# Kernel tuning notes

Measured on AMD Instinct MI355X. Metric: run time of the kernel, lower is better.

Reference implementation:

```python
import jax, jax.numpy as jnp
import numpy as np

DIM = 1280
HEADS = 16
HEAD_DIM = DIM // HEADS  # 80
N_CHUNKS = 8
CHUNK = 1024
TOTAL = N_CHUNKS * CHUNK  # 8192 packed tokens


def rotate_half(x):
    x1, x2 = jnp.split(x, 2, axis=-1)
    return jnp.concatenate([-x2, x1], axis=-1)


def setup_inputs() -> dict:
    key = jax.random.key(0)
    k0, k1, k2 = jax.random.split(key, 3)
    hidden_states = jax.random.normal(k0, (TOTAL, DIM), dtype=jnp.float32)
    # 2D-rope style per-token angles, duplicated halves (standard vision RoPE layout)
    inv_freq = 1.0 / (10000.0 ** (jnp.arange(0, HEAD_DIM, 2, dtype=jnp.float32) / HEAD_DIM))
    pos = jnp.arange(TOTAL, dtype=jnp.float32)
    freqs = pos[:, None] * inv_freq[None, :]            # [T, HEAD_DIM//2]
    emb = jnp.concatenate([freqs, freqs], axis=-1)      # [T, HEAD_DIM]
    cos = jnp.cos(emb)
    sin = jnp.sin(emb)
    qkv_w = jax.random.normal(k1, (3 * DIM, DIM), dtype=jnp.float32) * 0.02
    qkv_b = jnp.zeros((3 * DIM,), dtype=jnp.float32)
    proj_w = jax.random.normal(k2, (DIM, DIM), dtype=jnp.float32) * 0.02
    proj_b = jnp.zeros((DIM,), dtype=jnp.float32)
    cu_seqlens = (jnp.arange(N_CHUNKS + 1, dtype=jnp.int32) * CHUNK)
    return {"hidden_states": hidden_states, "cos": cos, "sin": sin,
            "qkv_w": qkv_w, "qkv_b": qkv_b, "proj_w": proj_w, "proj_b": proj_b,
            "cu_seqlens": cu_seqlens}


def reference(hidden_states, cos, sin, qkv_w, qkv_b, proj_w, proj_b, cu_seqlens):
    # Equal-length chunks (cu_seqlens uniform): vectorize the Python chunk loop
    # as a leading batch axis n over chunks of length L.
    n = cu_seqlens.shape[0] - 1
    total, dim = hidden_states.shape
    L = total // n
    scaling = HEAD_DIM ** -0.5

    x = hidden_states.reshape(n, L, dim)
    qkv = x @ qkv_w.T + qkv_b                              # [n, L, 3*dim]
    qkv = qkv.reshape(n, L, 3, HEADS, HEAD_DIM)
    q, k, v = qkv[:, :, 0], qkv[:, :, 1], qkv[:, :, 2]     # [n, L, H, hd]

    # inline RoPE in fp32 (matches apply_rotary_pos_emb_vision)
    c = cos.reshape(n, L, 1, HEAD_DIM).astype(jnp.float32)
    s = sin.reshape(n, L, 1, HEAD_DIM).astype(jnp.float32)
    qf = q.astype(jnp.float32)
    kf = k.astype(jnp.float32)
    q = (qf * c + rotate_half(qf) * s).astype(q.dtype)
    k = (kf * c + rotate_half(kf) * s).astype(k.dtype)

    # naive per-chunk full attention: QK^T, fp32 softmax, PV
    scores = jnp.einsum('nlhd,nmhd->nhlm', q, k) * scaling  # [n, H, L, L]
    probs = jax.nn.softmax(scores.astype(jnp.float32), axis=-1).astype(q.dtype)
    out = jnp.einsum('nhlm,nmhd->nlhd', probs, v)           # [n, L, H, hd]
    out = out.reshape(n, L, dim)
    out = out @ proj_w.T + proj_b                           # [n, L, dim]
    return out.reshape(total, dim)
```

## Files before the change

kernel.cpp:

```cpp
#include <hip/hip_runtime.h>
#include <stdint.h>

#define DIM 1280
#define HEADS 16
#define HD 80
#define TOTAL 8192
#define CHUNK 1024
#define QKVN 3840

typedef __attribute__((ext_vector_type(8))) __bf16 bf16x8;
typedef __attribute__((ext_vector_type(4))) float floatx4;

typedef __attribute__((address_space(1))) const uint32_t gu32;
typedef __attribute__((address_space(3))) uint32_t lu32;

__device__ __forceinline__ void llds16(const void* g, void* l) {
  __builtin_amdgcn_global_load_lds((gu32*)g, (lu32*)l, 16, 0, 0);
}

__device__ __forceinline__ unsigned short f2b(float f) {
  union { __bf16 b; unsigned short u; } x; x.b = (__bf16)f; return x.u;
}
__device__ __forceinline__ float b2f(unsigned short u) {
  union { __bf16 b; unsigned short u; } x; x.u = u; return (float)x.b;
}
__device__ __forceinline__ float fexp2(float x) {
#if __has_builtin(__builtin_amdgcn_exp2f)
  return __builtin_amdgcn_exp2f(x);
#else
  return __expf(x * 0.6931471805599453f);
#endif
}

#define QSCALE (0.11180339887498949f * 1.44269504088896340f)

#define QROW 96
#define KT_SH (64 * 104)
#define VT_SH (80 * 72)

__global__ void cvt_bf16(const float* __restrict__ src, unsigned short* __restrict__ dst, int n4) {
  int i = blockIdx.x * 256 + threadIdx.x;
  if (i >= n4) return;
  float4 v = reinterpret_cast<const float4*>(src)[i];
  ushort4 o;
  o.x = f2b(v.x); o.y = f2b(v.y); o.z = f2b(v.z); o.w = f2b(v.w);
  reinterpret_cast<ushort4*>(dst)[i] = o;
}


__device__ __forceinline__ void stage_a64(const unsigned short* __restrict__ G,
                                          unsigned short* ls, int wv, int lane,
                                          int row0, int kk, int hi) {
#pragma unroll
  for (int t = 0; t < 2; ++t) {
    const int stripe = t * 8 + wv;
    const int rb = ((stripe >> 3) << 7) + ((stripe & 7) << 3) + hi;
    const int r = rb + (lane >> 3);
    const int ch = (lane & 7) ^ (r & 7);
    llds16(G + (size_t)(row0 + r) * DIM + kk + (ch << 3), ls + rb * 64);
  }
}

__device__ __forceinline__ void stage_b64(const unsigned short* __restrict__ G,
                                          unsigned short* ls, int wv, int lane,
                                          int row0, int kk, int hi) {
#pragma unroll
  for (int t = 0; t < 2; ++t) {
    const int stripe = t * 8 + wv;
    const int rb = ((stripe >> 2) << 6) + ((stripe & 3) << 3) + hi;
    const int r = rb + (lane >> 3);
    const int ch = (lane & 7) ^ (r & 7);
    llds16(G + (size_t)(row0 + r) * DIM + kk + (ch << 3), ls + rb * 64);
  }
}

__device__ __forceinline__ bf16x8 frg(const unsigned short* ls, int r, int cx) {
  return *reinterpret_cast<const bf16x8*>(ls + r * 64 + (cx << 3));
}

#define MFMA_BF16 __builtin_amdgcn_mfma_f32_16x16x32_bf16
#define LGKM0() asm volatile("s_waitcnt lgkmcnt(0)" ::: "memory")
#define BARR()  asm volatile("s_barrier" ::: "memory")

template<int MODE>
__launch_bounds__(512, 2)
__global__ void gemm8(const unsigned short* __restrict__ A,
                      const unsigned short* __restrict__ B,
                      const float* __restrict__ bias,
                      unsigned short* __restrict__ qo,
                      unsigned short* __restrict__ ko,
                      unsigned short* __restrict__ vo,
                      float* __restrict__ fo) {
  __shared__ __attribute__((aligned(16))) unsigned short lsA[2][256 * 64];
  __shared__ __attribute__((aligned(16))) unsigned short lsB[2][256 * 64];
  const int m0 = blockIdx.x * 256;
  const int n0 = blockIdx.y * 256;
  const int tid = threadIdx.x;
  const int wv = tid >> 6, lane = tid & 63;
  const int wr = wv >> 2, wc = wv & 3;
  const int q4 = lane >> 4, l15 = lane & 15;
  const int sx = l15 & 7;
  const int cx0 = q4 ^ sx;
  const int cx1 = (4 + q4) ^ sx;

  stage_a64(A, &lsA[0][0], wv, lane, m0, 0, 0);
  stage_b64(B, &lsB[0][0], wv, lane, n0, 0, 0);
  stage_b64(B, &lsB[0][0], wv, lane, n0, 0, 32);
  stage_a64(A, &lsA[0][0], wv, lane, m0, 0, 64);
  stage_b64(B, &lsB[1][0], wv, lane, n0, 64, 0);
  stage_a64(A, &lsA[1][0], wv, lane, m0, 64, 0);
  stage_b64(B, &lsB[1][0], wv, lane, n0, 64, 32);

  floatx4 acc[8][4];
#pragma unroll
  for (int i = 0; i < 8; ++i)
#pragma unroll
    for (int j = 0; j < 4; ++j)
      acc[i][j] = (floatx4){0.f, 0.f, 0.f, 0.f};

  asm volatile("s_waitcnt vmcnt(6)" ::: "memory");
  BARR();

  const int rA = wr * 128 + l15;
  const int rB = wc * 64 + l15;

  bf16x8 ArLo[4][2], ArHi[4][2], Blo[2][2], Bhi[2][2];

#pragma unroll 2
  for (int kt = 0; kt < 20; ++kt) {
    const unsigned short* la = &lsA[kt & 1][0];
    const unsigned short* lb = &lsB[kt & 1][0];
    unsigned short* aN = &lsA[(kt & 1) ^ 1][0];
    unsigned short* aC = &lsA[kt & 1][0];
    unsigned short* bC = &lsB[kt & 1][0];
    const bool st1 = (kt + 1 < 20);
    const bool st2 = (kt + 2 < 20);

    if (kt > 0) {
#pragma unroll
      for (int m = 0; m < 4; ++m)
#pragma unroll
        for (int n = 0; n < 2; ++n) {
          acc[m + 4][n] = MFMA_BF16(ArHi[m][0], Blo[n][0], acc[m + 4][n], 0, 0, 0);
          acc[m + 4][n] = MFMA_BF16(ArHi[m][1], Blo[n][1], acc[m + 4][n], 0, 0, 0);
        }
    }
#pragma unroll
    for (int m = 0; m < 4; ++m) {
      ArLo[m][0] = frg(la, rA + m * 16, cx0);
      ArLo[m][1] = frg(la, rA + m * 16, cx1);
    }
#pragma unroll
    for (int n = 0; n < 2; ++n) {
      Blo[n][0] = frg(lb, rB + n * 16, cx0);
      Blo[n][1] = frg(lb, rB + n * 16, cx1);
    }
    if (st1) stage_a64(A, aN, wv, lane, m0, (kt + 1) * 64, 64);
    LGKM0();
    BARR();

#pragma unroll
    for (int m = 0; m < 4; ++m)
#pragma unroll
      for (int n = 0; n < 2; ++n) {
        acc[m][n] = MFMA_BF16(ArLo[m][0], Blo[n][0], acc[m][n], 0, 0, 0);
        acc[m][n] = MFMA_BF16(ArLo[m][1], Blo[n][1], acc[m][n], 0, 0, 0);
      }
#pragma unroll
    for (int n = 0; n < 2; ++n) {
      Bhi[n][0] = frg(lb, rB + (n + 2) * 16, cx0);
      Bhi[n][1] = frg(lb, rB + (n + 2) * 16, cx1);
    }
    if (st2) stage_b64(B, bC, wv, lane, n0, (kt + 2) * 64, 0);
    LGKM0();
    BARR();

#pragma unroll
    for (int m = 0; m < 4; ++m)
#pragma unroll
      for (int n = 0; n < 2; ++n) {
        acc[m][n + 2] = MFMA_BF16(ArLo[m][0], Bhi[n][0], acc[m][n + 2], 0, 0, 0);
        acc[m][n + 2] = MFMA_BF16(ArLo[m][1], Bhi[n][1], acc[m][n + 2], 0, 0, 0);
      }
#pragma unroll
    for (int m = 0; m < 4; ++m) {
      ArHi[m][0] = frg(la, rA + (m + 4) * 16, cx0);
      ArHi[m][1] = frg(la, rA + (m + 4) * 16, cx1);
    }
    if (st2) stage_a64(A, aC, wv, lane, m0, (kt + 2) * 64, 0);
    LGKM0();
    BARR();

#pragma unroll
    for (int m = 0; m < 4; ++m)
#pragma unroll
      for (int n = 0; n < 2; ++n) {
        acc[m + 4][n + 2] = MFMA_BF16(ArHi[m][0], Bhi[n][0], acc[m + 4][n + 2], 0, 0, 0);
        acc[m + 4][n + 2] = MFMA_BF16(ArHi[m][1], Bhi[n][1], acc[m + 4][n + 2], 0, 0, 0);
      }
    if (st2) stage_b64(B, bC, wv, lane, n0, (kt + 2) * 64, 32);
    if (st2)      asm volatile("s_waitcnt vmcnt(6)" ::: "memory");
    else if (st1) asm volatile("s_waitcnt vmcnt(0)" ::: "memory");
    BARR();
  }

#pragma unroll
  for (int m = 0; m < 4; ++m)
#pragma unroll
    for (int n = 0; n < 2; ++n) {
      acc[m + 4][n] = MFMA_BF16(ArHi[m][0], Blo[n][0], acc[m + 4][n], 0, 0, 0);
      acc[m + 4][n] = MFMA_BF16(ArHi[m][1], Blo[n][1], acc[m + 4][n], 0, 0, 0);
    }

  unsigned short* os = nullptr;
  int nloc = n0;
  if (MODE == 0) {
    if (blockIdx.y < 5)       { os = qo; }
    else if (blockIdx.y < 10) { os = ko; nloc = n0 - DIM; }
    else                      { os = vo; nloc = n0 - 2 * DIM; }
  }
#pragma unroll
  for (int n = 0; n < 4; ++n) {
    const int cg = wc * 64 + n * 16 + l15;
    const float bn = bias[n0 + cg];
#pragma unroll
    for (int m = 0; m < 8; ++m) {
#pragma unroll
      for (int r = 0; r < 4; ++r) {
        const int row = m0 + wr * 128 + m * 16 + q4 * 4 + r;
        const float val = acc[m][n][r] + bn;
        if (MODE == 0) os[(size_t)row * DIM + nloc + cg] = f2b(val);
        else           fo[(size_t)row * DIM + n0 + cg] = val;
      }
    }
  }
}

__global__ void prep_q(const unsigned short* __restrict__ qbuf,
                       const float* __restrict__ cp, const float* __restrict__ sp,
                       unsigned short* __restrict__ qimg) {
  const int m = blockIdx.x, tid = threadIdx.x;
  const int ch = m >> 10, rl = m & 1023;
#pragma unroll
  for (int i = 0; i < 3; ++i) {
    const int it = i * 256 + tid;
    if (it < 640) {
      const int h = it / 40, d = it - h * 40;
      const float c = cp[m * HD + d], s = sp[m * HD + d];
      const float x1 = b2f(qbuf[(size_t)m * DIM + h * HD + d]);
      const float x2 = b2f(qbuf[(size_t)m * DIM + h * HD + d + 40]);
      const size_t ob = ((size_t)(ch * 16 + h) * 1024 + rl) * QROW;
      qimg[ob + d]      = f2b((x1 * c - x2 * s) * QSCALE);
      qimg[ob + d + 40] = f2b((x2 * c + x1 * s) * QSCALE);
    }
  }
  { const int h = tid >> 4, c = tid & 15;
    qimg[((size_t)(ch * 16 + h) * 1024 + rl) * QROW + 80 + c] = 0; }
}

__global__ void prep_k(const unsigned short* __restrict__ kbuf,
                       const float* __restrict__ cp, const float* __restrict__ sp,
                       unsigned short* __restrict__ kimg) {
  const int m = blockIdx.x, tid = threadIdx.x;
  const int ch = m >> 10, rl = m & 1023;
  const int jt = rl >> 6, rr = rl & 63;
#pragma unroll
  for (int i = 0; i < 3; ++i) {
    const int it = i * 256 + tid;
    if (it < 640) {
      const int h = it / 40, d = it - h * 40;
      const float c = cp[m * HD + d], s = sp[m * HD + d];
      const float x1 = b2f(kbuf[(size_t)m * DIM + h * HD + d]);
      const float x2 = b2f(kbuf[(size_t)m * DIM + h * HD + d + 40]);
      const size_t ob = ((size_t)((ch * 16 + h) * 16 + jt) * KT_SH) + rr * 104;
      kimg[ob + d]      = f2b(x1 * c - x2 * s);
      kimg[ob + d + 40] = f2b(x2 * c + x1 * s);
    }
  }
#pragma unroll
  for (int i = 0; i < 2; ++i) {
    const int it = i * 256 + tid;
    if (it < 384) {
      const int h = it / 24, c = it - h * 24;
      kimg[((size_t)((ch * 16 + h) * 16 + jt) * KT_SH) + rr * 104 + 80 + c] = 0;
    }
  }
}

__global__ void prep_v(const unsigned short* __restrict__ vbuf,
                       unsigned short* __restrict__ vimg) {
  __shared__ __attribute__((aligned(16))) unsigned short lsT[64 * 88];
  const int bx = blockIdx.x;
  const int jt = bx & 15, h = (bx >> 4) & 15, ch = bx >> 8;
  const int tid = threadIdx.x;
  const int row0 = ch * CHUNK + jt * 64;
#pragma unroll
  for (int i = 0; i < 3; ++i) {
    const int it = i * 256 + tid;
    if (it < 640) {
      const int r = it / 10, c = it - r * 10;
      const uint4 v = *reinterpret_cast<const uint4*>(vbuf + (size_t)(row0 + r) * DIM + h * HD + c * 8);
      *reinterpret_cast<uint4*>(&lsT[r * 88 + c * 8]) = v;
    }
  }
  __syncthreads();
  unsigned short* ot = vimg + (size_t)((ch * 16 + h) * 16 + jt) * VT_SH;
#pragma unroll
  for (int i = 0; i < 12; ++i) {
    const int it = i * 256 + tid;
    if (it < 2880) {
      const int d = it / 36, kk = it - d * 36;
      uint32_t w = 0;
      if (kk < 32) {
        const uint32_t lo = lsT[(2 * kk) * 88 + d];
        const uint32_t hi = lsT[(2 * kk + 1) * 88 + d];
        w = lo | (hi << 16);
      }
      *reinterpret_cast<uint32_t*>(ot + d * 72 + kk * 2) = w;
    }
  }
}

__launch_bounds__(256, 3)
__global__ void attn_k(const unsigned short* __restrict__ qimg,
                       const unsigned short* __restrict__ kimg,
                       const unsigned short* __restrict__ vimg,
                       unsigned short* __restrict__ ob) {
  __shared__ __attribute__((aligned(16))) unsigned short lsK[KT_SH];
  __shared__ __attribute__((aligned(16))) unsigned short lsV[VT_SH];
  __shared__ __attribute__((aligned(16))) unsigned short lsP[128 * 72];

  const int bx = blockIdx.x;
  const int qt = bx & 7, h = (bx >> 3) & 15, ch = bx >> 7;
  const int tid = threadIdx.x, wv = tid >> 6, lane = tid & 63;
  const int q4 = lane >> 4, l15 = lane & 15;
  const int qrow_loc = qt * 128 + wv * 32;

  bf16x8 aq[2][3];
  {
    const unsigned short* qb = qimg + ((size_t)(ch * 16 + h) * 1024 + qrow_loc) * QROW;
#pragma unroll
    for (int mt = 0; mt < 2; ++mt)
#pragma unroll
      for (int ks = 0; ks < 3; ++ks)
        aq[mt][ks] = *reinterpret_cast<const bf16x8*>(qb + (size_t)(mt * 16 + l15) * QROW + ks * 32 + q4 * 8);
  }

  floatx4 oacc[2][5];
  float lpart[2] = {0.f, 0.f};
#pragma unroll
  for (int mt = 0; mt < 2; ++mt)
#pragma unroll
    for (int t = 0; t < 5; ++t) oacc[mt][t] = (floatx4){0.f, 0.f, 0.f, 0.f};

  const char* kbase = (const char*)(kimg + (size_t)(ch * 16 + h) * 16 * KT_SH);
  const char* vbase = (const char*)(vimg + (size_t)(ch * 16 + h) * 16 * VT_SH);

  for (int jt = 0; jt < 16; ++jt) {
    __syncthreads();
    {
      const char* kg = kbase + (size_t)jt * (KT_SH * 2);
#pragma unroll
      for (int r = 0; r < 4; ++r) {
        const int off = (r * 4 + wv) * 1024;
        if (off < KT_SH * 2)
          llds16(kg + off + lane * 16, (char*)lsK + off);
      }
      const char* vg = vbase + (size_t)jt * (VT_SH * 2);
#pragma unroll
      for (int r = 0; r < 3; ++r) {
        const int off = (r * 4 + wv) * 1024;
        if (off < VT_SH * 2) {
          if (off + 1024 <= VT_SH * 2) llds16(vg + off + lane * 16, (char*)lsV + off);
          else if (lane < 16)          llds16(vg + off + lane * 16, (char*)lsV + off);
        }
      }
    }
    __syncthreads();

    floatx4 sfr[2][4];
#pragma unroll
    for (int c = 0; c < 4; ++c) {
      const bf16x8 ak0 = *reinterpret_cast<const bf16x8*>(&lsK[(c * 16 + l15) * 104 + 0  + q4 * 8]);
      const bf16x8 ak1 = *reinterpret_cast<const bf16x8*>(&lsK[(c * 16 + l15) * 104 + 32 + q4 * 8]);
      const bf16x8 ak2 = *reinterpret_cast<const bf16x8*>(&lsK[(c * 16 + l15) * 104 + 64 + q4 * 8]);
#pragma unroll
      for (int mt = 0; mt < 2; ++mt) {
        floatx4 s = (floatx4){0.f, 0.f, 0.f, 0.f};
        s = __builtin_amdgcn_mfma_f32_16x16x32_bf16(ak0, aq[mt][0], s, 0, 0, 0);
        s = __builtin_amdgcn_mfma_f32_16x16x32_bf16(ak1, aq[mt][1], s, 0, 0, 0);
        s = __builtin_amdgcn_mfma_f32_16x16x32_bf16(ak2, aq[mt][2], s, 0, 0, 0);
        sfr[mt][c] = s;
      }
    }

#pragma unroll
    for (int mt = 0; mt < 2; ++mt)
#pragma unroll
      for (int c = 0; c < 4; ++c) {
        const float p0 = fexp2(sfr[mt][c][0]);
        const float p1 = fexp2(sfr[mt][c][1]);
        const float p2 = fexp2(sfr[mt][c][2]);
        const float p3 = fexp2(sfr[mt][c][3]);
        lpart[mt] += (p0 + p1) + (p2 + p3);
        ushort4 w;
        w.x = f2b(p0); w.y = f2b(p1); w.z = f2b(p2); w.w = f2b(p3);
        *reinterpret_cast<ushort4*>(&lsP[(wv * 32 + mt * 16 + l15) * 72 + c * 16 + q4 * 4]) = w;
      }

#pragma unroll
    for (int ks = 0; ks < 2; ++ks) {
      const bf16x8 ap0 = *reinterpret_cast<const bf16x8*>(&lsP[(wv * 32 + 0  + l15) * 72 + ks * 32 + q4 * 8]);
      const bf16x8 ap1 = *reinterpret_cast<const bf16x8*>(&lsP[(wv * 32 + 16 + l15) * 72 + ks * 32 + q4 * 8]);
#pragma unroll
      for (int t = 0; t < 5; ++t) {
        const bf16x8 bv = *reinterpret_cast<const bf16x8*>(&lsV[(t * 16 + l15) * 72 + ks * 32 + q4 * 8]);
        oacc[0][t] = __builtin_amdgcn_mfma_f32_16x16x32_bf16(ap0, bv, oacc[0][t], 0, 0, 0);
        oacc[1][t] = __builtin_amdgcn_mfma_f32_16x16x32_bf16(ap1, bv, oacc[1][t], 0, 0, 0);
      }
    }
  }

#pragma unroll
  for (int mt = 0; mt < 2; ++mt) {
    lpart[mt] += __shfl_xor(lpart[mt], 16, 64);
    lpart[mt] += __shfl_xor(lpart[mt], 32, 64);
  }
  float inv[2];
  inv[0] = 1.0f / lpart[0];
  inv[1] = 1.0f / lpart[1];

  float invr[2][4];
#pragma unroll
  for (int mt = 0; mt < 2; ++mt)
#pragma unroll
    for (int r = 0; r < 4; ++r)
      invr[mt][r] = __shfl(inv[mt], q4 * 4 + r, 64);

#pragma unroll
  for (int mt = 0; mt < 2; ++mt)
#pragma unroll
    for (int t = 0; t < 5; ++t)
#pragma unroll
      for (int r = 0; r < 4; ++r) {
        const int gr = ch * CHUNK + qrow_loc + mt * 16 + q4 * 4 + r;
        const int gc = h * HD + t * 16 + l15;
        ob[(size_t)gr * DIM + gc] = f2b(oacc[mt][t][r] * invr[mt][r]);
      }
}

extern "C" void kernel_launch(void* const* d_in, const int* in_sizes, int n_in,
                              void* d_out, int out_size, void* d_ws, size_t ws_size,
                              hipStream_t stream) {
  (void)in_sizes; (void)n_in; (void)out_size; (void)ws_size;
  const float* hs    = (const float*)d_in[0];
  const float* cosp  = (const float*)d_in[1];
  const float* sinp  = (const float*)d_in[2];
  const float* qkvw  = (const float*)d_in[3];
  const float* qkvb  = (const float*)d_in[4];
  const float* projw = (const float*)d_in[5];
  const float* projb = (const float*)d_in[6];

  char* ws = (char*)d_ws;
  unsigned short* xb   = (unsigned short*)(ws + 0);
  unsigned short* wq   = (unsigned short*)(ws + 20971520);
  unsigned short* qbuf = (unsigned short*)(ws + 30801920);
  unsigned short* kbuf = (unsigned short*)(ws + 51773440);
  unsigned short* vbuf = (unsigned short*)(ws + 72744960);
  unsigned short* wp   = (unsigned short*)(ws + 93716480);
  unsigned short* obuf = (unsigned short*)(ws + 96993280);
  unsigned short* kimg = (unsigned short*)(ws + 117964800);
  unsigned short* qimg = (unsigned short*)(ws + 0);
  unsigned short* vimg = (unsigned short*)(ws + 30801920);

  cvt_bf16<<<TOTAL * DIM / 4 / 256, 256, 0, stream>>>(hs, xb, TOTAL * DIM / 4);
  cvt_bf16<<<QKVN * DIM / 4 / 256, 256, 0, stream>>>(qkvw, wq, QKVN * DIM / 4);
  cvt_bf16<<<DIM * DIM / 4 / 256, 256, 0, stream>>>(projw, wp, DIM * DIM / 4);

  gemm8<0><<<dim3(TOTAL / 256, QKVN / 256), 512, 0, stream>>>(
      xb, wq, qkvb, qbuf, kbuf, vbuf, nullptr);

  prep_q<<<TOTAL, 256, 0, stream>>>(qbuf, cosp, sinp, qimg);
  prep_k<<<TOTAL, 256, 0, stream>>>(kbuf, cosp, sinp, kimg);
  prep_v<<<2048, 256, 0, stream>>>(vbuf, vimg);

  attn_k<<<1024, 256, 0, stream>>>(qimg, kimg, vimg, obuf);

  gemm8<1><<<dim3(TOTAL / 256, DIM / 256), 512, 0, stream>>>(
      obuf, wp, projb, nullptr, nullptr, nullptr, (float*)d_out);
}
```

Baseline: 351.4 us.

## Double-buffer K/V tiles in attention and raise wave priority around MFMAs

The attention kernel now keeps two LDS buffers for K and V. It issues the async global-to-LDS load for the next key tile right after the barrier, then computes on the current tile, and drops the second barrier per iteration. MFMA sections are wrapped in s_setprio to favour matrix issue. The doubled LDS footprint lowers the launch-bounds occupancy hint from 3 to 2 blocks. The compiler may also insert conservative vmcnt waits before the LDS reads, which would cancel much of the intended overlap.

```diff
diff --git a/kernel.cpp b/kernel.cpp
--- a/kernel.cpp
+++ b/kernel.cpp
@@ -321,13 +321,13 @@
   }
 }
 
-__launch_bounds__(256, 3)
+__launch_bounds__(256, 2)
 __global__ void attn_k(const unsigned short* __restrict__ qimg,
                        const unsigned short* __restrict__ kimg,
                        const unsigned short* __restrict__ vimg,
                        unsigned short* __restrict__ ob) {
-  __shared__ __attribute__((aligned(16))) unsigned short lsK[KT_SH];
-  __shared__ __attribute__((aligned(16))) unsigned short lsV[VT_SH];
+  __shared__ __attribute__((aligned(16))) unsigned short lsK[2][KT_SH];
+  __shared__ __attribute__((aligned(16))) unsigned short lsV[2][VT_SH];
   __shared__ __attribute__((aligned(16))) unsigned short lsP[128 * 72];
 
   const int bx = blockIdx.x;
@@ -356,34 +356,43 @@
   const char* kbase = (const char*)(kimg + (size_t)(ch * 16 + h) * 16 * KT_SH);
   const char* vbase = (const char*)(vimg + (size_t)(ch * 16 + h) * 16 * VT_SH);
 
+  auto stage_kv = [&](int jt, char* lk, char* lv) {
+    const char* kg = kbase + (size_t)jt * (KT_SH * 2);
+#pragma unroll
+    for (int r = 0; r < 4; ++r) {
+      const int off = (r * 4 + wv) * 1024;
+      if (off < KT_SH * 2)
+        llds16(kg + off + lane * 16, lk + off);
+    }
+    const char* vg = vbase + (size_t)jt * (VT_SH * 2);
+#pragma unroll
+    for (int r = 0; r < 3; ++r) {
+      const int off = (r * 4 + wv) * 1024;
+      if (off < VT_SH * 2) {
+        if (off + 1024 <= VT_SH * 2) llds16(vg + off + lane * 16, lv + off);
+        else if (lane < 16)          llds16(vg + off + lane * 16, lv + off);
+      }
+    }
+  };
+
+  stage_kv(0, (char*)lsK[0], (char*)lsV[0]);
+
   for (int jt = 0; jt < 16; ++jt) {
+    const int cur = jt & 1;
     __syncthreads();
-    {
-      const char* kg = kbase + (size_t)jt * (KT_SH * 2);
-#pragma unroll
-      for (int r = 0; r < 4; ++r) {
-        const int off = (r * 4 + wv) * 1024;
-        if (off < KT_SH * 2)
-          llds16(kg + off + lane * 16, (char*)lsK + off);
-      }
-      const char* vg = vbase + (size_t)jt * (VT_SH * 2);
-#pragma unroll
-      for (int r = 0; r < 3; ++r) {
-        const int off = (r * 4 + wv) * 1024;
-        if (off < VT_SH * 2) {
-          if (off + 1024 <= VT_SH * 2) llds16(vg + off + lane * 16, (char*)lsV + off);
-          else if (lane < 16)          llds16(vg + off + lane * 16, (char*)lsV + off);
-        }
-      }
-    }
-    __syncthreads();
+    if (jt + 1 < 16)
+      stage_kv(jt + 1, (char*)lsK[cur ^ 1], (char*)lsV[cur ^ 1]);
+
+    const unsigned short* lk = lsK[cur];
+    const unsigned short* lv = lsV[cur];
 
     floatx4 sfr[2][4];
+    __builtin_amdgcn_s_setprio(1);
 #pragma unroll
     for (int c = 0; c < 4; ++c) {
-      const bf16x8 ak0 = *reinterpret_cast<const bf16x8*>(&lsK[(c * 16 + l15) * 104 + 0  + q4 * 8]);
-      const bf16x8 ak1 = *reinterpret_cast<const bf16x8*>(&lsK[(c * 16 + l15) * 104 + 32 + q4 * 8]);
-      const bf16x8 ak2 = *reinterpret_cast<const bf16x8*>(&lsK[(c * 16 + l15) * 104 + 64 + q4 * 8]);
+      const bf16x8 ak0 = *reinterpret_cast<const bf16x8*>(&lk[(c * 16 + l15) * 104 + 0  + q4 * 8]);
+      const bf16x8 ak1 = *reinterpret_cast<const bf16x8*>(&lk[(c * 16 + l15) * 104 + 32 + q4 * 8]);
+      const bf16x8 ak2 = *reinterpret_cast<const bf16x8*>(&lk[(c * 16 + l15) * 104 + 64 + q4 * 8]);
 #pragma unroll
       for (int mt = 0; mt < 2; ++mt) {
         floatx4 s = (floatx4){0.f, 0.f, 0.f, 0.f};
@@ -393,6 +402,7 @@
         sfr[mt][c] = s;
       }
     }
+    __builtin_amdgcn_s_setprio(0);
 
 #pragma unroll
     for (int mt = 0; mt < 2; ++mt)
@@ -408,17 +418,19 @@
         *reinterpret_cast<ushort4*>(&lsP[(wv * 32 + mt * 16 + l15) * 72 + c * 16 + q4 * 4]) = w;
       }
 
+    __builtin_amdgcn_s_setprio(1);
 #pragma unroll
     for (int ks = 0; ks < 2; ++ks) {
       const bf16x8 ap0 = *reinterpret_cast<const bf16x8*>(&lsP[(wv * 32 + 0  + l15) * 72 + ks * 32 + q4 * 8]);
       const bf16x8 ap1 = *reinterpret_cast<const bf16x8*>(&lsP[(wv * 32 + 16 + l15) * 72 + ks * 32 + q4 * 8]);
 #pragma unroll
       for (int t = 0; t < 5; ++t) {
-        const bf16x8 bv = *reinterpret_cast<const bf16x8*>(&lsV[(t * 16 + l15) * 72 + ks * 32 + q4 * 8]);
+        const bf16x8 bv = *reinterpret_cast<const bf16x8*>(&lv[(t * 16 + l15) * 72 + ks * 32 + q4 * 8]);
         oacc[0][t] = __builtin_amdgcn_mfma_f32_16x16x32_bf16(ap0, bv, oacc[0][t], 0, 0, 0);
         oacc[1][t] = __builtin_amdgcn_mfma_f32_16x16x32_bf16(ap1, bv, oacc[1][t], 0, 0, 0);
       }
     }
+    __builtin_amdgcn_s_setprio(0);
   }
 
 #pragma unroll
```

New measurement: 352.2 us. Within noise of the previous version (+0.2%).
